# Optimization experiments

Hardware: AMD Instinct MI355X
Metric: run time of the kernel (lower is better)

## Reference

```python
import jax, jax.numpy as jnp
import numpy as np

B, S, D, L = 64, 512, 256, 3
NUM_BUCKETS = 1500  # RelativePositionBias default


def _ln(x, g, b):
    m = x.mean(-1, keepdims=True)
    v = x.var(-1, keepdims=True)
    return (x - m) * jax.lax.rsqrt(v + 1e-5) * g + b


def setup_inputs() -> dict:
    key = jax.random.key(0)
    ks = jax.random.split(key, 10)
    s = 0.02
    f32 = jnp.float32
    return dict(
        x=jax.random.normal(ks[0], (B, S, D), f32),
        mask=jnp.ones((B, S), jnp.int32),
        bias_table=jax.random.normal(ks[1], (NUM_BUCKETS,), f32) * s,  # n_heads=1
        ln_g=jnp.ones((L, D), f32), ln_b=jnp.zeros((L, D), f32),
        wq=jax.random.normal(ks[2], (L, D, D), f32) * s, bq=jnp.zeros((L, D), f32),
        wk=jax.random.normal(ks[3], (L, D, D), f32) * s, bk=jnp.zeros((L, D), f32),
        wv=jax.random.normal(ks[4], (L, D, D), f32) * s, bv=jnp.zeros((L, D), f32),
        wo=jax.random.normal(ks[5], (L, D, D), f32) * s, bo=jnp.zeros((L, D), f32),
        cm_ln_g=jnp.ones((L, D), f32), cm_ln_b=jnp.zeros((L, D), f32),
        w1=jax.random.normal(ks[6], (L, D, D), f32) * s, b1=jnp.zeros((L, D), f32),
        w2=jax.random.normal(ks[7], (L, D, D), f32) * s, b2=jnp.zeros((L, D), f32),
    )


def reference(x, mask, bias_table, ln_g, ln_b, wq, bq, wk, bk, wv, bv, wo, bo,
              cm_ln_g, cm_ln_b, w1, b1, w2, b2):
    slen = x.shape[1]
    # relative position bias (RelativePositionBias.compute_bias), n_heads=1
    pos = jnp.arange(slen)
    rel = pos[None, :] - pos[:, None]        # memory - context
    maxn = slen - 1                          # torch.max(rel)
    bucket = jnp.where(rel < 0, -rel + maxn, rel)
    cp = bias_table[bucket]                  # [S, S], broadcasts over batch
    scale = jnp.sqrt(jnp.asarray(x.shape[-1], x.dtype))  # sqrt(hid_dim // 1)
    pad = (mask == 0)[:, None, :]            # [B, 1, S] key-side padding mask
    neg = jnp.finfo(x.dtype).min
    for j in range(L):
        h = _ln(x, ln_g[j], ln_b[j])
        q = h @ wq[j] + bq[j]
        k = h @ wk[j] + bk[j]
        v = h @ wv[j] + bv[j]
        e = jnp.einsum('bqd,bkd->bqk', q, k) / scale + cp
        e = jnp.where(pad, neg, e)
        a = jax.nn.softmax(e, axis=-1)
        o = jnp.einsum('bqk,bkd->bqd', a, v) @ wo[j] + bo[j]
        x = h + _ln(o, ln_g[j], ln_b[j])     # same LayerNorm reused, per source
        c = _ln(x, cm_ln_g[j], cm_ln_b[j])
        x = x + (jax.nn.gelu(c @ w1[j] + b1[j], approximate=False) @ w2[j] + b2[j])
    return x
```

## Files before the change

kernel.cpp:

```cpp
#include <hip/hip_runtime.h>
#include <hip/hip_bf16.h>
#include <math.h>

#define D_HID 256
#define N_B   64
#define S_LEN 512
#define N_L   3
#define M_ROWS (N_B * S_LEN)

typedef __bf16 bf16_t;
typedef __bf16 bf16x8 __attribute__((ext_vector_type(8)));
typedef __bf16 bf16x4 __attribute__((ext_vector_type(4)));
typedef float  f32x4  __attribute__((ext_vector_type(4)));
typedef unsigned int u32;

__device__ __forceinline__ f32x4 mfma16(bf16x8 a, bf16x8 b, f32x4 c) {
    return __builtin_amdgcn_mfma_f32_16x16x32_bf16(a, b, c, 0, 0, 0);
}

__device__ __forceinline__ void gld_lds16(const void* g, void* l) {
    __builtin_amdgcn_global_load_lds((const __attribute__((address_space(1))) u32*)g,
                                     (__attribute__((address_space(3))) u32*)l, 16, 0, 0);
}

__device__ __forceinline__ u32 pk_bf16(float a, float b) {
    return (u32)(__hip_bfloat16_raw(__hip_bfloat16(a)).x) |
           ((u32)(__hip_bfloat16_raw(__hip_bfloat16(b)).x) << 16);
}

__global__ __launch_bounds__(256) void transpose_all(const float* __restrict__ wq,
                                                     const float* __restrict__ wk,
                                                     const float* __restrict__ wv,
                                                     const float* __restrict__ wo,
                                                     const float* __restrict__ w1,
                                                     const float* __restrict__ w2,
                                                     bf16_t* __restrict__ Wqkv,
                                                     bf16_t* __restrict__ Wrest) {
    const int t = blockIdx.y;
    const float* src = t == 0 ? wq : t == 1 ? wk : t == 2 ? wv
                     : t == 3 ? wo : t == 4 ? w1 : w2;
    const int i = blockIdx.x * 256 + threadIdx.x;
    const int k = i & 255;
    const int n = (i >> 8) & 255;
    const int l = i >> 16;
    const bf16_t v = (bf16_t)src[((size_t)l << 16) + ((size_t)k << 8) + n];
    if (t < 3) Wqkv[(size_t)l * 3 * 65536 + t * 65536 + n * 256 + k] = v;
    else       Wrest[(size_t)(t - 3) * 196608 + l * 65536 + n * 256 + k] = v;
}

__global__ __launch_bounds__(256) void ln_fwd(const float* __restrict__ in,
                                              const float* __restrict__ g,
                                              const float* __restrict__ b,
                                              float* __restrict__ H,
                                              bf16_t* __restrict__ Hb) {
    int row  = blockIdx.x * 4 + (threadIdx.x >> 6);
    int lane = threadIdx.x & 63;
    float4 x = ((const float4*)(in + (size_t)row * D_HID))[lane];
    float s  = x.x + x.y + x.z + x.w;
    float sq = x.x * x.x + x.y * x.y + x.z * x.z + x.w * x.w;
#pragma unroll
    for (int o = 1; o < 64; o <<= 1) { s += __shfl_xor(s, o); sq += __shfl_xor(sq, o); }
    float mean = s * (1.f / D_HID);
    float rstd = rsqrtf(sq * (1.f / D_HID) - mean * mean + 1e-5f);
    float4 gv = ((const float4*)g)[lane];
    float4 bv = ((const float4*)b)[lane];
    float4 h;
    h.x = (x.x - mean) * rstd * gv.x + bv.x;
    h.y = (x.y - mean) * rstd * gv.y + bv.y;
    h.z = (x.z - mean) * rstd * gv.z + bv.z;
    h.w = (x.w - mean) * rstd * gv.w + bv.w;
    ((float4*)(H + (size_t)row * D_HID))[lane] = h;
    bf16x4 hb = { (bf16_t)h.x, (bf16_t)h.y, (bf16_t)h.z, (bf16_t)h.w };
    *((bf16x4*)(Hb + (size_t)row * D_HID) + lane) = hb;
}

__global__ __launch_bounds__(256) void ln_res_ln(const float* __restrict__ T,
                                                 const float* __restrict__ H,
                                                 const float* __restrict__ g,
                                                 const float* __restrict__ b,
                                                 const float* __restrict__ cg,
                                                 const float* __restrict__ cb,
                                                 float* __restrict__ X,
                                                 bf16_t* __restrict__ Cb) {
    int row  = blockIdx.x * 4 + (threadIdx.x >> 6);
    int lane = threadIdx.x & 63;
    float4 t = ((const float4*)(T + (size_t)row * D_HID))[lane];
    float s  = t.x + t.y + t.z + t.w;
    float sq = t.x * t.x + t.y * t.y + t.z * t.z + t.w * t.w;
#pragma unroll
    for (int o = 1; o < 64; o <<= 1) { s += __shfl_xor(s, o); sq += __shfl_xor(sq, o); }
    float mean = s * (1.f / D_HID);
    float rstd = rsqrtf(sq * (1.f / D_HID) - mean * mean + 1e-5f);
    float4 gv = ((const float4*)g)[lane];
    float4 bv = ((const float4*)b)[lane];
    float4 hh = ((const float4*)(H + (size_t)row * D_HID))[lane];
    float4 x;
    x.x = hh.x + (t.x - mean) * rstd * gv.x + bv.x;
    x.y = hh.y + (t.y - mean) * rstd * gv.y + bv.y;
    x.z = hh.z + (t.z - mean) * rstd * gv.z + bv.z;
    x.w = hh.w + (t.w - mean) * rstd * gv.w + bv.w;
    ((float4*)(X + (size_t)row * D_HID))[lane] = x;
    float s2  = x.x + x.y + x.z + x.w;
    float sq2 = x.x * x.x + x.y * x.y + x.z * x.z + x.w * x.w;
#pragma unroll
    for (int o = 1; o < 64; o <<= 1) { s2 += __shfl_xor(s2, o); sq2 += __shfl_xor(sq2, o); }
    float mean2 = s2 * (1.f / D_HID);
    float rstd2 = rsqrtf(sq2 * (1.f / D_HID) - mean2 * mean2 + 1e-5f);
    float4 cgv = ((const float4*)cg)[lane];
    float4 cbv = ((const float4*)cb)[lane];
    bf16x4 c = { (bf16_t)((x.x - mean2) * rstd2 * cgv.x + cbv.x),
                 (bf16_t)((x.y - mean2) * rstd2 * cgv.y + cbv.y),
                 (bf16_t)((x.z - mean2) * rstd2 * cgv.z + cbv.z),
                 (bf16_t)((x.w - mean2) * rstd2 * cgv.w + cbv.w) };
    *((bf16x4*)(Cb + (size_t)row * D_HID) + lane) = c;
}

__device__ __forceinline__ void stage_tile(const bf16_t* __restrict__ A,
                                           const bf16_t* __restrict__ W,
                                           int m0, int n0, int kt,
                                           bf16_t* As, bf16_t* Bs) {
    const int lane = threadIdx.x & 63;
    const int wid  = threadIdx.x >> 6;
#pragma unroll
    for (int i = 0; i < 4; ++i) {
        const int base8 = i * 256 + wid * 64;
        const int idx8  = base8 + lane;
        const int row   = idx8 >> 3;
        const int sc8   = (idx8 & 7) ^ (row & 7);
        gld_lds16(A + (size_t)(m0 + row) * D_HID + kt * 64 + sc8 * 8, As + base8 * 8);
        gld_lds16(W + (size_t)(n0 + row) * D_HID + kt * 64 + sc8 * 8, Bs + base8 * 8);
    }
}

__device__ __forceinline__ void compute_tile(const bf16_t* As, const bf16_t* Bs,
                                             f32x4 (&acc)[4][4]) {
    const int lane = threadIdx.x & 63;
    const int wid  = threadIdx.x >> 6;
    const int wm = wid >> 1, wn = wid & 1;
    const int r = lane & 15, g = lane >> 4;
#pragma unroll
    for (int ks = 0; ks < 2; ++ks) {
        bf16x8 af[4], bfr[4];
#pragma unroll
        for (int mt = 0; mt < 4; ++mt) {
            const int row = wm * 64 + mt * 16 + r;
            const int c8  = (ks * 4 + g) ^ (row & 7);
            af[mt] = *(const bf16x8*)(As + row * 64 + c8 * 8);
        }
#pragma unroll
        for (int nt = 0; nt < 4; ++nt) {
            const int row = wn * 64 + nt * 16 + r;
            const int c8  = (ks * 4 + g) ^ (row & 7);
            bfr[nt] = *(const bf16x8*)(Bs + row * 64 + c8 * 8);
        }
#pragma unroll
        for (int mt = 0; mt < 4; ++mt)
#pragma unroll
            for (int nt = 0; nt < 4; ++nt)
                acc[mt][nt] = mfma16(af[mt], bfr[nt], acc[mt][nt]);
    }
}

__device__ __forceinline__ void gemm_core(const bf16_t* __restrict__ A,
                                          const bf16_t* __restrict__ W,
                                          int m0, int n0,
                                          bf16_t (&As)[2][8192], bf16_t (&Bs)[2][8192],
                                          f32x4 (&acc)[4][4]) {
    stage_tile(A, W, m0, n0, 0, As[0], Bs[0]);
    asm volatile("s_waitcnt vmcnt(0)" ::: "memory");
    __builtin_amdgcn_s_barrier();
#pragma unroll
    for (int kt = 0; kt < 4; ++kt) {
        const int cur = kt & 1;
        if (kt < 3) stage_tile(A, W, m0, n0, kt + 1, As[cur ^ 1], Bs[cur ^ 1]);
        compute_tile(As[cur], Bs[cur], acc);
        if (kt < 3) {
            asm volatile("s_waitcnt vmcnt(0)" ::: "memory");
            __builtin_amdgcn_s_barrier();
        }
    }
}

__global__ __launch_bounds__(256) void gemm_qkv(const bf16_t* __restrict__ A,
                                                const bf16_t* __restrict__ Wp,
                                                const float* __restrict__ bq,
                                                const float* __restrict__ bk,
                                                const float* __restrict__ bv,
                                                bf16_t* __restrict__ Qb,
                                                bf16_t* __restrict__ Kb,
                                                bf16_t* __restrict__ Vt) {
    __shared__ bf16_t As[2][8192], Bs[2][8192];
    f32x4 acc[4][4] = {};
    const int m0 = blockIdx.x * 128, n0 = blockIdx.y * 128;
    gemm_core(A, Wp, m0, n0, As, Bs, acc);
    const int lane = threadIdx.x & 63, wid = threadIdx.x >> 6;
    const int wm = wid >> 1, wn = wid & 1, r = lane & 15, g = lane >> 4;
#pragma unroll
    for (int nt = 0; nt < 4; ++nt) {
        const int col = n0 + wn * 64 + nt * 16 + r;
        const int t = col >> 8, cc = col & 255;
        const float bias = (t == 0 ? bq : t == 1 ? bk : bv)[cc];
#pragma unroll
        for (int mt = 0; mt < 4; ++mt)
#pragma unroll
            for (int rr = 0; rr < 4; ++rr) {
                const int row = m0 + wm * 64 + mt * 16 + g * 4 + rr;
                const float v = acc[mt][nt][rr] + bias;
                if (t == 0)      Qb[(size_t)row * D_HID + cc] = (bf16_t)v;
                else if (t == 1) Kb[(size_t)row * D_HID + cc] = (bf16_t)v;
                else             Vt[((size_t)(row >> 9) * D_HID + cc) * S_LEN + (row & 511)] = (bf16_t)v;
            }
    }
}

template <int EPI>
__global__ __launch_bounds__(256) void gemm_one(const bf16_t* __restrict__ A,
                                                const bf16_t* __restrict__ W,
                                                const float* __restrict__ bias,
                                                void* __restrict__ outp,
                                                const float* __restrict__ addsrc) {
    __shared__ bf16_t As[2][8192], Bs[2][8192];
    f32x4 acc[4][4] = {};
    const int m0 = blockIdx.x * 128, n0 = blockIdx.y * 128;
    gemm_core(A, W, m0, n0, As, Bs, acc);
    const int lane = threadIdx.x & 63, wid = threadIdx.x >> 6;
    const int wm = wid >> 1, wn = wid & 1, r = lane & 15, g = lane >> 4;
#pragma unroll
    for (int nt = 0; nt < 4; ++nt) {
        const int col = n0 + wn * 64 + nt * 16 + r;
        const float bv = bias[col];
#pragma unroll
        for (int mt = 0; mt < 4; ++mt)
#pragma unroll
            for (int rr = 0; rr < 4; ++rr) {
                const size_t idx = (size_t)(m0 + wm * 64 + mt * 16 + g * 4 + rr) * D_HID + col;
                float v = acc[mt][nt][rr] + bv;
                if constexpr (EPI == 1) {
                    v = 0.5f * v * (1.f + erff(v * 0.70710678118654752f));
                    ((bf16_t*)outp)[idx] = (bf16_t)v;
                } else if constexpr (EPI == 2) {
                    ((float*)outp)[idx] = v;
                } else {
                    ((float*)outp)[idx] = addsrc[idx] + v;
                }
            }
    }
}

__global__ __launch_bounds__(256, 2) void attn_fwd(const bf16_t* __restrict__ Q,
                                                   const bf16_t* __restrict__ K,
                                                   const bf16_t* __restrict__ Vt,
                                                   const float* __restrict__ btab,
                                                   const int* __restrict__ mask,
                                                   bf16_t* __restrict__ AO) {
    __shared__ float  bias_lds[1024];
    __shared__ float  mask_add[512];
    __shared__ bf16_t P_lds[32 * 64];
    __shared__ float  m_part[4][32], l_part[4][32];
    __shared__ bf16_t o_lds[32][264];

    const int tid = threadIdx.x, lane = tid & 63, w = tid >> 6;
    const int r = lane & 15, g = lane >> 4;

    const int lid = blockIdx.x;
    const int xcd = lid & 7, slot = lid >> 3;
    const int b  = xcd * 8 + (slot >> 4);
    const int q0 = (slot & 15) * 32;

    for (int i = tid; i < 1024; i += 256) {
        const int rel = i - 512;
        const int bucket = (rel < 0) ? (511 - rel) : rel;
        bias_lds[i] = btab[bucket];
    }
    for (int i = tid; i < 512; i += 256)
        mask_add[i] = mask[b * S_LEN + i] ? 0.f : -3.0e38f;
    __syncthreads();

    const bf16_t* Qp = Q  + ((size_t)b * S_LEN + q0) * D_HID;
    const bf16_t* Kp = K  + (size_t)b * S_LEN * D_HID;
    const bf16_t* Vp = Vt + (size_t)b * D_HID * S_LEN;

    bf16x8 qf[2][8];
#pragma unroll
    for (int ks = 0; ks < 8; ++ks) {
        qf[0][ks] = *(const bf16x8*)(Qp + (size_t)r * D_HID + ks * 32 + g * 8);
        qf[1][ks] = *(const bf16x8*)(Qp + (size_t)(16 + r) * D_HID + ks * 32 + g * 8);
    }

    f32x4 oacc[4][2] = {};
    float m_run[2] = {-3.0e38f, -3.0e38f};
    float l_run[2] = {0.f, 0.f};

#pragma unroll 1
    for (int kt = 0; kt < 8; ++kt) {
        const int k0 = kt * 64;
        bf16x8 vpre[2][4];
#pragma unroll
        for (int ks = 0; ks < 2; ++ks)
#pragma unroll
            for (int nt = 0; nt < 4; ++nt)
                vpre[ks][nt] = *(const bf16x8*)(Vp + (size_t)(w * 64 + nt * 16 + r) * S_LEN
                                                     + k0 + ks * 32 + g * 8);
        f32x4 sacc[2] = {};
#pragma unroll
        for (int ks = 0; ks < 8; ++ks) {
            const int dk = ks * 32 + g * 8;
            bf16x8 kf = *(const bf16x8*)(Kp + (size_t)(k0 + w * 16 + r) * D_HID + dk);
            sacc[0] = mfma16(kf, qf[0][ks], sacc[0]);
            sacc[1] = mfma16(kf, qf[1][ks], sacc[1]);
        }
        float mx[2] = {-3.0e38f, -3.0e38f};
#pragma unroll
        for (int qb = 0; qb < 2; ++qb) {
            const int qg = q0 + qb * 16 + r;
#pragma unroll
            for (int rr = 0; rr < 4; ++rr) {
                const int kg = k0 + w * 16 + g * 4 + rr;
                float ev = sacc[qb][rr] * 0.0625f + bias_lds[kg - qg + 512] + mask_add[kg];
                sacc[qb][rr] = ev;
                mx[qb] = fmaxf(mx[qb], ev);
            }
            mx[qb] = fmaxf(mx[qb], __shfl_xor(mx[qb], 16));
            mx[qb] = fmaxf(mx[qb], __shfl_xor(mx[qb], 32));
        }
        if (g == 0) { m_part[w][r] = mx[0]; m_part[w][16 + r] = mx[1]; }
        __syncthreads();
        float mnew[2], fac[2];
#pragma unroll
        for (int qb = 0; qb < 2; ++qb) {
            const int q = qb * 16 + r;
            const float tm = fmaxf(fmaxf(m_part[0][q], m_part[1][q]),
                                   fmaxf(m_part[2][q], m_part[3][q]));
            mnew[qb] = fmaxf(m_run[qb], tm);
            fac[qb]  = __expf(m_run[qb] - mnew[qb]);
            m_run[qb] = mnew[qb];
        }
#pragma unroll
        for (int qb = 0; qb < 2; ++qb) {
            const float p0 = __expf(sacc[qb][0] - mnew[qb]);
            const float p1 = __expf(sacc[qb][1] - mnew[qb]);
            const float p2 = __expf(sacc[qb][2] - mnew[qb]);
            const float p3 = __expf(sacc[qb][3] - mnew[qb]);
            float ls = p0 + p1 + p2 + p3;
            ls += __shfl_xor(ls, 16);
            ls += __shfl_xor(ls, 32);
            if (g == 0) l_part[w][qb * 16 + r] = ls;
            const int q = qb * 16 + r;
            const int u = (2 * w + (g >> 1)) ^ (q & 7);
            uint2 pv; pv.x = pk_bf16(p0, p1); pv.y = pk_bf16(p2, p3);
            *(uint2*)((char*)P_lds + q * 128 + u * 16 + (g & 1) * 8) = pv;
        }
        __syncthreads();
#pragma unroll
        for (int qb = 0; qb < 2; ++qb) {
            const int q = qb * 16 + r;
            const float lt = l_part[0][q] + l_part[1][q] + l_part[2][q] + l_part[3][q];
            l_run[qb] = l_run[qb] * fac[qb] + lt;
        }
#pragma unroll
        for (int nt = 0; nt < 4; ++nt)
#pragma unroll
            for (int qb = 0; qb < 2; ++qb)
#pragma unroll
                for (int rr = 0; rr < 4; ++rr)
                    oacc[nt][qb][rr] *= fac[qb];
#pragma unroll
        for (int ks = 0; ks < 2; ++ks) {
            bf16x8 pf[2];
#pragma unroll
            for (int qb = 0; qb < 2; ++qb) {
                const int q = qb * 16 + r;
                const int u = (ks * 4 + g) ^ (q & 7);
                pf[qb] = *(const bf16x8*)((const char*)P_lds + q * 128 + u * 16);
            }
            __builtin_amdgcn_s_setprio(1);
#pragma unroll
            for (int nt = 0; nt < 4; ++nt) {
                oacc[nt][0] = mfma16(vpre[ks][nt], pf[0], oacc[nt][0]);
                oacc[nt][1] = mfma16(vpre[ks][nt], pf[1], oacc[nt][1]);
            }
            __builtin_amdgcn_s_setprio(0);
        }
    }
    const float inv_l[2] = { 1.f / fmaxf(l_run[0], 1e-30f),
                             1.f / fmaxf(l_run[1], 1e-30f) };
#pragma unroll
    for (int nt = 0; nt < 4; ++nt)
#pragma unroll
        for (int qb = 0; qb < 2; ++qb) {
            const int q = qb * 16 + r;
            const int d = w * 64 + nt * 16 + g * 4;
            bf16x4 ob = { (bf16_t)(oacc[nt][qb][0] * inv_l[qb]),
                          (bf16_t)(oacc[nt][qb][1] * inv_l[qb]),
                          (bf16_t)(oacc[nt][qb][2] * inv_l[qb]),
                          (bf16_t)(oacc[nt][qb][3] * inv_l[qb]) };
            *(bf16x4*)&o_lds[q][d] = ob;
        }
    __syncthreads();
    bf16_t* Op = AO + ((size_t)b * S_LEN + q0) * D_HID;
#pragma unroll
    for (int it = 0; it < 4; ++it) {
        const int idx = it * 256 + tid;
        const int row = idx >> 5, u = idx & 31;
        bf16x8 vv = *(const bf16x8*)&o_lds[row][u * 8];
        *(bf16x8*)(Op + (size_t)row * D_HID + u * 8) = vv;
    }
}

extern "C" void kernel_launch(void* const* d_in, const int* in_sizes, int n_in,
                              void* d_out, int out_size, void* d_ws, size_t ws_size,
                              hipStream_t stream) {
    const float* x_in = (const float*)d_in[0];
    const int*   mask = (const int*)d_in[1];
    const float* btab = (const float*)d_in[2];
    const float* ln_g = (const float*)d_in[3];
    const float* ln_b = (const float*)d_in[4];
    const float* wq = (const float*)d_in[5];
    const float* bq = (const float*)d_in[6];
    const float* wk = (const float*)d_in[7];
    const float* bk = (const float*)d_in[8];
    const float* wv = (const float*)d_in[9];
    const float* bv = (const float*)d_in[10];
    const float* wo = (const float*)d_in[11];
    const float* bo = (const float*)d_in[12];
    const float* cg = (const float*)d_in[13];
    const float* cb = (const float*)d_in[14];
    const float* w1 = (const float*)d_in[15];
    const float* b1 = (const float*)d_in[16];
    const float* w2 = (const float*)d_in[17];
    const float* b2 = (const float*)d_in[18];
    float* out = (float*)d_out;

    char* p = (char*)d_ws;
    const size_t F32SZ  = (size_t)M_ROWS * D_HID * sizeof(float);
    const size_t BF16SZ = (size_t)M_ROWS * D_HID * sizeof(bf16_t);
    float*  H  = (float*)p;  p += F32SZ;
    float*  X  = (float*)p;  p += F32SZ;
    bf16_t* Hb = (bf16_t*)p; p += BF16SZ;
    bf16_t* Qb = (bf16_t*)p; p += BF16SZ;
    bf16_t* Kb = (bf16_t*)p;
    float*  T  = (float*)Kb;
    bf16_t* T1b = Kb;
    p += BF16SZ;
    bf16_t* Vt = (bf16_t*)p; p += BF16SZ;
    bf16_t* Wqkv = (bf16_t*)p; p += (size_t)N_L * 768 * 256 * sizeof(bf16_t);
    bf16_t* Wrest = (bf16_t*)p;
    bf16_t* AO = Hb;
    bf16_t* Cb = Qb;

    transpose_all<<<dim3(768, 6), dim3(256), 0, stream>>>(wq, wk, wv, wo, w1, w2, Wqkv, Wrest);

    const dim3 gblk(256, 1, 1);
    const dim3 grid_qkv(M_ROWS / 128, 6, 1);
    const dim3 grid_one(M_ROWS / 128, 2, 1);

    for (int j = 0; j < N_L; ++j) {
        const bf16_t* WQKVj = Wqkv + (size_t)j * 3 * 65536;
        const bf16_t* WOt = Wrest + ((size_t)0 * N_L + j) * 65536;
        const bf16_t* W1t = Wrest + ((size_t)1 * N_L + j) * 65536;
        const bf16_t* W2t = Wrest + ((size_t)2 * N_L + j) * 65536;

        ln_fwd<<<dim3(M_ROWS / 4), gblk, 0, stream>>>(j == 0 ? x_in : X,
                                                      ln_g + j * D_HID, ln_b + j * D_HID, H, Hb);
        gemm_qkv<<<grid_qkv, gblk, 0, stream>>>(Hb, WQKVj, bq + j * D_HID, bk + j * D_HID,
                                                bv + j * D_HID, Qb, Kb, Vt);
        attn_fwd<<<dim3(N_B * 16, 1, 1), gblk, 0, stream>>>(Qb, Kb, Vt, btab, mask, AO);
        gemm_one<2><<<grid_one, gblk, 0, stream>>>(AO, WOt, bo + j * D_HID, T, nullptr);
        ln_res_ln<<<dim3(M_ROWS / 4), gblk, 0, stream>>>(T, H, ln_g + j * D_HID, ln_b + j * D_HID,
                                                         cg + j * D_HID, cb + j * D_HID, X, Cb);
        gemm_one<1><<<grid_one, gblk, 0, stream>>>(Cb, W1t, b1 + j * D_HID, T1b, nullptr);
        gemm_one<3><<<grid_one, gblk, 0, stream>>>(T1b, W2t, b2 + j * D_HID,
                                                   (j == N_L - 1) ? (void*)out : (void*)X, X);
    }
}
```

Baseline: 687.7 us.

## Shrink GEMM and attention tiles and drop fp32 LayerNorm residual copy

GEMM block tiles shrink from 128x128 to 64x128, and attention blocks now cover 16 query rows instead of 32. Both changes double the grid size and lower per-block registers and LDS, aiming for better occupancy and load balance. The fp32 H buffer is removed: the residual now reads the bf16 LayerNorm output, which cuts memory traffic but adds rounding error to the residual path. AO gets its own buffer because Hb is still needed later for the residual. Attention blocks now reuse each K/V tile across fewer queries, so K/V reads from global memory double.

```diff
diff --git a/kernel.cpp b/kernel.cpp
--- a/kernel.cpp
+++ b/kernel.cpp
@@ -51,7 +51,6 @@
 __global__ __launch_bounds__(256) void ln_fwd(const float* __restrict__ in,
                                               const float* __restrict__ g,
                                               const float* __restrict__ b,
-                                              float* __restrict__ H,
                                               bf16_t* __restrict__ Hb) {
     int row  = blockIdx.x * 4 + (threadIdx.x >> 6);
     int lane = threadIdx.x & 63;
@@ -64,18 +63,15 @@
     float rstd = rsqrtf(sq * (1.f / D_HID) - mean * mean + 1e-5f);
     float4 gv = ((const float4*)g)[lane];
     float4 bv = ((const float4*)b)[lane];
-    float4 h;
-    h.x = (x.x - mean) * rstd * gv.x + bv.x;
-    h.y = (x.y - mean) * rstd * gv.y + bv.y;
-    h.z = (x.z - mean) * rstd * gv.z + bv.z;
-    h.w = (x.w - mean) * rstd * gv.w + bv.w;
-    ((float4*)(H + (size_t)row * D_HID))[lane] = h;
-    bf16x4 hb = { (bf16_t)h.x, (bf16_t)h.y, (bf16_t)h.z, (bf16_t)h.w };
+    bf16x4 hb = { (bf16_t)((x.x - mean) * rstd * gv.x + bv.x),
+                  (bf16_t)((x.y - mean) * rstd * gv.y + bv.y),
+                  (bf16_t)((x.z - mean) * rstd * gv.z + bv.z),
+                  (bf16_t)((x.w - mean) * rstd * gv.w + bv.w) };
     *((bf16x4*)(Hb + (size_t)row * D_HID) + lane) = hb;
 }
 
 __global__ __launch_bounds__(256) void ln_res_ln(const float* __restrict__ T,
-                                                 const float* __restrict__ H,
+                                                 const bf16_t* __restrict__ Hb,
                                                  const float* __restrict__ g,
                                                  const float* __restrict__ b,
                                                  const float* __restrict__ cg,
@@ -93,12 +89,12 @@
     float rstd = rsqrtf(sq * (1.f / D_HID) - mean * mean + 1e-5f);
     float4 gv = ((const float4*)g)[lane];
     float4 bv = ((const float4*)b)[lane];
-    float4 hh = ((const float4*)(H + (size_t)row * D_HID))[lane];
+    bf16x4 hb = *((const bf16x4*)(Hb + (size_t)row * D_HID) + lane);
     float4 x;
-    x.x = hh.x + (t.x - mean) * rstd * gv.x + bv.x;
-    x.y = hh.y + (t.y - mean) * rstd * gv.y + bv.y;
-    x.z = hh.z + (t.z - mean) * rstd * gv.z + bv.z;
-    x.w = hh.w + (t.w - mean) * rstd * gv.w + bv.w;
+    x.x = (float)hb[0] + (t.x - mean) * rstd * gv.x + bv.x;
+    x.y = (float)hb[1] + (t.y - mean) * rstd * gv.y + bv.y;
+    x.z = (float)hb[2] + (t.z - mean) * rstd * gv.z + bv.z;
+    x.w = (float)hb[3] + (t.w - mean) * rstd * gv.w + bv.w;
     ((float4*)(X + (size_t)row * D_HID))[lane] = x;
     float s2  = x.x + x.y + x.z + x.w;
     float sq2 = x.x * x.x + x.y * x.y + x.z * x.z + x.w * x.w;
@@ -122,28 +118,35 @@
     const int lane = threadIdx.x & 63;
     const int wid  = threadIdx.x >> 6;
 #pragma unroll
+    for (int i = 0; i < 2; ++i) {
+        const int base8 = i * 256 + wid * 64;
+        const int idx8  = base8 + lane;
+        const int row   = idx8 >> 3;
+        const int sc8   = (idx8 & 7) ^ (row & 7);
+        gld_lds16(A + (size_t)(m0 + row) * D_HID + kt * 64 + sc8 * 8, As + base8 * 8);
+    }
+#pragma unroll
     for (int i = 0; i < 4; ++i) {
         const int base8 = i * 256 + wid * 64;
         const int idx8  = base8 + lane;
         const int row   = idx8 >> 3;
         const int sc8   = (idx8 & 7) ^ (row & 7);
-        gld_lds16(A + (size_t)(m0 + row) * D_HID + kt * 64 + sc8 * 8, As + base8 * 8);
         gld_lds16(W + (size_t)(n0 + row) * D_HID + kt * 64 + sc8 * 8, Bs + base8 * 8);
     }
 }
 
 __device__ __forceinline__ void compute_tile(const bf16_t* As, const bf16_t* Bs,
-                                             f32x4 (&acc)[4][4]) {
+                                             f32x4 (&acc)[2][4]) {
     const int lane = threadIdx.x & 63;
     const int wid  = threadIdx.x >> 6;
     const int wm = wid >> 1, wn = wid & 1;
     const int r = lane & 15, g = lane >> 4;
 #pragma unroll
     for (int ks = 0; ks < 2; ++ks) {
-        bf16x8 af[4], bfr[4];
-#pragma unroll
-        for (int mt = 0; mt < 4; ++mt) {
-            const int row = wm * 64 + mt * 16 + r;
+        bf16x8 af[2], bfr[4];
+#pragma unroll
+        for (int mt = 0; mt < 2; ++mt) {
+            const int row = wm * 32 + mt * 16 + r;
             const int c8  = (ks * 4 + g) ^ (row & 7);
             af[mt] = *(const bf16x8*)(As + row * 64 + c8 * 8);
         }
@@ -154,7 +157,7 @@
             bfr[nt] = *(const bf16x8*)(Bs + row * 64 + c8 * 8);
         }
 #pragma unroll
-        for (int mt = 0; mt < 4; ++mt)
+        for (int mt = 0; mt < 2; ++mt)
 #pragma unroll
             for (int nt = 0; nt < 4; ++nt)
                 acc[mt][nt] = mfma16(af[mt], bfr[nt], acc[mt][nt]);
@@ -164,8 +167,8 @@
 __device__ __forceinline__ void gemm_core(const bf16_t* __restrict__ A,
                                           const bf16_t* __restrict__ W,
                                           int m0, int n0,
-                                          bf16_t (&As)[2][8192], bf16_t (&Bs)[2][8192],
-                                          f32x4 (&acc)[4][4]) {
+                                          bf16_t (&As)[2][4096], bf16_t (&Bs)[2][8192],
+                                          f32x4 (&acc)[2][4]) {
     stage_tile(A, W, m0, n0, 0, As[0], Bs[0]);
     asm volatile("s_waitcnt vmcnt(0)" ::: "memory");
     __builtin_amdgcn_s_barrier();
@@ -189,9 +192,9 @@
                                                 bf16_t* __restrict__ Qb,
                                                 bf16_t* __restrict__ Kb,
                                                 bf16_t* __restrict__ Vt) {
-    __shared__ bf16_t As[2][8192], Bs[2][8192];
-    f32x4 acc[4][4] = {};
-    const int m0 = blockIdx.x * 128, n0 = blockIdx.y * 128;
+    __shared__ bf16_t As[2][4096], Bs[2][8192];
+    f32x4 acc[2][4] = {};
+    const int m0 = blockIdx.x * 64, n0 = blockIdx.y * 128;
     gemm_core(A, Wp, m0, n0, As, Bs, acc);
     const int lane = threadIdx.x & 63, wid = threadIdx.x >> 6;
     const int wm = wid >> 1, wn = wid & 1, r = lane & 15, g = lane >> 4;
@@ -201,10 +204,10 @@
         const int t = col >> 8, cc = col & 255;
         const float bias = (t == 0 ? bq : t == 1 ? bk : bv)[cc];
 #pragma unroll
-        for (int mt = 0; mt < 4; ++mt)
+        for (int mt = 0; mt < 2; ++mt)
 #pragma unroll
             for (int rr = 0; rr < 4; ++rr) {
-                const int row = m0 + wm * 64 + mt * 16 + g * 4 + rr;
+                const int row = m0 + wm * 32 + mt * 16 + g * 4 + rr;
                 const float v = acc[mt][nt][rr] + bias;
                 if (t == 0)      Qb[(size_t)row * D_HID + cc] = (bf16_t)v;
                 else if (t == 1) Kb[(size_t)row * D_HID + cc] = (bf16_t)v;
@@ -219,9 +222,9 @@
                                                 const float* __restrict__ bias,
                                                 void* __restrict__ outp,
                                                 const float* __restrict__ addsrc) {
-    __shared__ bf16_t As[2][8192], Bs[2][8192];
-    f32x4 acc[4][4] = {};
-    const int m0 = blockIdx.x * 128, n0 = blockIdx.y * 128;
+    __shared__ bf16_t As[2][4096], Bs[2][8192];
+    f32x4 acc[2][4] = {};
+    const int m0 = blockIdx.x * 64, n0 = blockIdx.y * 128;
     gemm_core(A, W, m0, n0, As, Bs, acc);
     const int lane = threadIdx.x & 63, wid = threadIdx.x >> 6;
     const int wm = wid >> 1, wn = wid & 1, r = lane & 15, g = lane >> 4;
@@ -230,10 +233,10 @@
         const int col = n0 + wn * 64 + nt * 16 + r;
         const float bv = bias[col];
 #pragma unroll
-        for (int mt = 0; mt < 4; ++mt)
+        for (int mt = 0; mt < 2; ++mt)
 #pragma unroll
             for (int rr = 0; rr < 4; ++rr) {
-                const size_t idx = (size_t)(m0 + wm * 64 + mt * 16 + g * 4 + rr) * D_HID + col;
+                const size_t idx = (size_t)(m0 + wm * 32 + mt * 16 + g * 4 + rr) * D_HID + col;
                 float v = acc[mt][nt][rr] + bv;
                 if constexpr (EPI == 1) {
                     v = 0.5f * v * (1.f + erff(v * 0.70710678118654752f));
@@ -255,17 +258,17 @@
                                                    bf16_t* __restrict__ AO) {
     __shared__ float  bias_lds[1024];
     __shared__ float  mask_add[512];
-    __shared__ bf16_t P_lds[32 * 64];
-    __shared__ float  m_part[4][32], l_part[4][32];
-    __shared__ bf16_t o_lds[32][264];
+    __shared__ bf16_t P_lds[16 * 64];
+    __shared__ float  m_part[4][16], l_part[4][16];
+    __shared__ bf16_t o_lds[16][264];
 
     const int tid = threadIdx.x, lane = tid & 63, w = tid >> 6;
     const int r = lane & 15, g = lane >> 4;
 
     const int lid = blockIdx.x;
     const int xcd = lid & 7, slot = lid >> 3;
-    const int b  = xcd * 8 + (slot >> 4);
-    const int q0 = (slot & 15) * 32;
+    const int b  = xcd * 8 + (slot >> 5);
+    const int q0 = (slot & 31) * 16;
 
     for (int i = tid; i < 1024; i += 256) {
         const int rel = i - 512;
@@ -280,16 +283,13 @@
     const bf16_t* Kp = K  + (size_t)b * S_LEN * D_HID;
     const bf16_t* Vp = Vt + (size_t)b * D_HID * S_LEN;
 
-    bf16x8 qf[2][8];
-#pragma unroll
-    for (int ks = 0; ks < 8; ++ks) {
-        qf[0][ks] = *(const bf16x8*)(Qp + (size_t)r * D_HID + ks * 32 + g * 8);
-        qf[1][ks] = *(const bf16x8*)(Qp + (size_t)(16 + r) * D_HID + ks * 32 + g * 8);
-    }
-
-    f32x4 oacc[4][2] = {};
-    float m_run[2] = {-3.0e38f, -3.0e38f};
-    float l_run[2] = {0.f, 0.f};
+    bf16x8 qf[8];
+#pragma unroll
+    for (int ks = 0; ks < 8; ++ks)
+        qf[ks] = *(const bf16x8*)(Qp + (size_t)r * D_HID + ks * 32 + g * 8);
+
+    f32x4 oacc[4] = {};
+    float m_run = -3.0e38f, l_run = 0.f;
 
 #pragma unroll 1
     for (int kt = 0; kt < 8; ++kt) {
@@ -301,105 +301,76 @@
             for (int nt = 0; nt < 4; ++nt)
                 vpre[ks][nt] = *(const bf16x8*)(Vp + (size_t)(w * 64 + nt * 16 + r) * S_LEN
                                                      + k0 + ks * 32 + g * 8);
-        f32x4 sacc[2] = {};
+        f32x4 sacc = {};
 #pragma unroll
         for (int ks = 0; ks < 8; ++ks) {
-            const int dk = ks * 32 + g * 8;
-            bf16x8 kf = *(const bf16x8*)(Kp + (size_t)(k0 + w * 16 + r) * D_HID + dk);
-            sacc[0] = mfma16(kf, qf[0][ks], sacc[0]);
-            sacc[1] = mfma16(kf, qf[1][ks], sacc[1]);
-        }
-        float mx[2] = {-3.0e38f, -3.0e38f};
-#pragma unroll
-        for (int qb = 0; qb < 2; ++qb) {
-            const int qg = q0 + qb * 16 + r;
-#pragma unroll
-            for (int rr = 0; rr < 4; ++rr) {
-                const int kg = k0 + w * 16 + g * 4 + rr;
-                float ev = sacc[qb][rr] * 0.0625f + bias_lds[kg - qg + 512] + mask_add[kg];
-                sacc[qb][rr] = ev;
-                mx[qb] = fmaxf(mx[qb], ev);
-            }
-            mx[qb] = fmaxf(mx[qb], __shfl_xor(mx[qb], 16));
-            mx[qb] = fmaxf(mx[qb], __shfl_xor(mx[qb], 32));
-        }
-        if (g == 0) { m_part[w][r] = mx[0]; m_part[w][16 + r] = mx[1]; }
+            bf16x8 kf = *(const bf16x8*)(Kp + (size_t)(k0 + w * 16 + r) * D_HID + ks * 32 + g * 8);
+            sacc = mfma16(kf, qf[ks], sacc);
+        }
+        float mx = -3.0e38f;
+        const int qg = q0 + r;
+#pragma unroll
+        for (int rr = 0; rr < 4; ++rr) {
+            const int kg = k0 + w * 16 + g * 4 + rr;
+            float ev = sacc[rr] * 0.0625f + bias_lds[kg - qg + 512] + mask_add[kg];
+            sacc[rr] = ev;
+            mx = fmaxf(mx, ev);
+        }
+        mx = fmaxf(mx, __shfl_xor(mx, 16));
+        mx = fmaxf(mx, __shfl_xor(mx, 32));
+        if (g == 0) m_part[w][r] = mx;
         __syncthreads();
-        float mnew[2], fac[2];
-#pragma unroll
-        for (int qb = 0; qb < 2; ++qb) {
-            const int q = qb * 16 + r;
-            const float tm = fmaxf(fmaxf(m_part[0][q], m_part[1][q]),
-                                   fmaxf(m_part[2][q], m_part[3][q]));
-            mnew[qb] = fmaxf(m_run[qb], tm);
-            fac[qb]  = __expf(m_run[qb] - mnew[qb]);
-            m_run[qb] = mnew[qb];
-        }
-#pragma unroll
-        for (int qb = 0; qb < 2; ++qb) {
-            const float p0 = __expf(sacc[qb][0] - mnew[qb]);
-            const float p1 = __expf(sacc[qb][1] - mnew[qb]);
-            const float p2 = __expf(sacc[qb][2] - mnew[qb]);
-            const float p3 = __expf(sacc[qb][3] - mnew[qb]);
-            float ls = p0 + p1 + p2 + p3;
-            ls += __shfl_xor(ls, 16);
-            ls += __shfl_xor(ls, 32);
-            if (g == 0) l_part[w][qb * 16 + r] = ls;
-            const int q = qb * 16 + r;
-            const int u = (2 * w + (g >> 1)) ^ (q & 7);
+        const float tm = fmaxf(fmaxf(m_part[0][r], m_part[1][r]),
+                               fmaxf(m_part[2][r], m_part[3][r]));
+        const float mnew = fmaxf(m_run, tm);
+        const float fac  = __expf(m_run - mnew);
+        m_run = mnew;
+        const float p0 = __expf(sacc[0] - mnew);
+        const float p1 = __expf(sacc[1] - mnew);
+        const float p2 = __expf(sacc[2] - mnew);
+        const float p3 = __expf(sacc[3] - mnew);
+        float ls = p0 + p1 + p2 + p3;
+        ls += __shfl_xor(ls, 16);
+        ls += __shfl_xor(ls, 32);
+        if (g == 0) l_part[w][r] = ls;
+        {
+            const int u = (2 * w + (g >> 1)) ^ (r & 7);
             uint2 pv; pv.x = pk_bf16(p0, p1); pv.y = pk_bf16(p2, p3);
-            *(uint2*)((char*)P_lds + q * 128 + u * 16 + (g & 1) * 8) = pv;
+            *(uint2*)((char*)P_lds + r * 128 + u * 16 + (g & 1) * 8) = pv;
         }
         __syncthreads();
-#pragma unroll
-        for (int qb = 0; qb < 2; ++qb) {
-            const int q = qb * 16 + r;
-            const float lt = l_part[0][q] + l_part[1][q] + l_part[2][q] + l_part[3][q];
-            l_run[qb] = l_run[qb] * fac[qb] + lt;
-        }
+        const float lt = l_part[0][r] + l_part[1][r] + l_part[2][r] + l_part[3][r];
+        l_run = l_run * fac + lt;
 #pragma unroll
         for (int nt = 0; nt < 4; ++nt)
 #pragma unroll
-            for (int qb = 0; qb < 2; ++qb)
-#pragma unroll
-                for (int rr = 0; rr < 4; ++rr)
-                    oacc[nt][qb][rr] *= fac[qb];
+            for (int rr = 0; rr < 4; ++rr)
+                oacc[nt][rr] *= fac;
 #pragma unroll
         for (int ks = 0; ks < 2; ++ks) {
-            bf16x8 pf[2];
-#pragma unroll
-            for (int qb = 0; qb < 2; ++qb) {
-                const int q = qb * 16 + r;
-                const int u = (ks * 4 + g) ^ (q & 7);
-                pf[qb] = *(const bf16x8*)((const char*)P_lds + q * 128 + u * 16);
-            }
+            const int u = (ks * 4 + g) ^ (r & 7);
+            bf16x8 pf = *(const bf16x8*)((const char*)P_lds + r * 128 + u * 16);
             __builtin_amdgcn_s_setprio(1);
 #pragma unroll
-            for (int nt = 0; nt < 4; ++nt) {
-                oacc[nt][0] = mfma16(vpre[ks][nt], pf[0], oacc[nt][0]);
-                oacc[nt][1] = mfma16(vpre[ks][nt], pf[1], oacc[nt][1]);
-            }
+            for (int nt = 0; nt < 4; ++nt)
+                oacc[nt] = mfma16(vpre[ks][nt], pf, oacc[nt]);
             __builtin_amdgcn_s_setprio(0);
         }
     }
-    const float inv_l[2] = { 1.f / fmaxf(l_run[0], 1e-30f),
-                             1.f / fmaxf(l_run[1], 1e-30f) };
-#pragma unroll
-    for (int nt = 0; nt < 4; ++nt)
-#pragma unroll
-        for (int qb = 0; qb < 2; ++qb) {
-            const int q = qb * 16 + r;
-            const int d = w * 64 + nt * 16 + g * 4;
-            bf16x4 ob = { (bf16_t)(oacc[nt][qb][0] * inv_l[qb]),
-                          (bf16_t)(oacc[nt][qb][1] * inv_l[qb]),
-                          (bf16_t)(oacc[nt][qb][2] * inv_l[qb]),
-                          (bf16_t)(oacc[nt][qb][3] * inv_l[qb]) };
-            *(bf16x4*)&o_lds[q][d] = ob;
-        }
+    const float inv_l = 1.f / fmaxf(l_run, 1e-30f);
+#pragma unroll
+    for (int nt = 0; nt < 4; ++nt) {
+        const int d = w * 64 + nt * 16 + g * 4;
+        bf16x4 ob = { (bf16_t)(oacc[nt][0] * inv_l),
+                      (bf16_t)(oacc[nt][1] * inv_l),
+                      (bf16_t)(oacc[nt][2] * inv_l),
+                      (bf16_t)(oacc[nt][3] * inv_l) };
+        *(bf16x4*)&o_lds[r][d] = ob;
+    }
     __syncthreads();
     bf16_t* Op = AO + ((size_t)b * S_LEN + q0) * D_HID;
 #pragma unroll
-    for (int it = 0; it < 4; ++it) {
+    for (int it = 0; it < 2; ++it) {
         const int idx = it * 256 + tid;
         const int row = idx >> 5, u = idx & 31;
         bf16x8 vv = *(const bf16x8*)&o_lds[row][u * 8];
@@ -434,7 +405,6 @@
     char* p = (char*)d_ws;
     const size_t F32SZ  = (size_t)M_ROWS * D_HID * sizeof(float);
     const size_t BF16SZ = (size_t)M_ROWS * D_HID * sizeof(bf16_t);
-    float*  H  = (float*)p;  p += F32SZ;
     float*  X  = (float*)p;  p += F32SZ;
     bf16_t* Hb = (bf16_t*)p; p += BF16SZ;
     bf16_t* Qb = (bf16_t*)p; p += BF16SZ;
@@ -443,16 +413,16 @@
     bf16_t* T1b = Kb;
     p += BF16SZ;
     bf16_t* Vt = (bf16_t*)p; p += BF16SZ;
+    bf16_t* AO = (bf16_t*)p; p += BF16SZ;
     bf16_t* Wqkv = (bf16_t*)p; p += (size_t)N_L * 768 * 256 * sizeof(bf16_t);
     bf16_t* Wrest = (bf16_t*)p;
-    bf16_t* AO = Hb;
     bf16_t* Cb = Qb;
 
     transpose_all<<<dim3(768, 6), dim3(256), 0, stream>>>(wq, wk, wv, wo, w1, w2, Wqkv, Wrest);
 
     const dim3 gblk(256, 1, 1);
-    const dim3 grid_qkv(M_ROWS / 128, 6, 1);
-    const dim3 grid_one(M_ROWS / 128, 2, 1);
+    const dim3 grid_qkv(M_ROWS / 64, 6, 1);
+    const dim3 grid_one(M_ROWS / 64, 2, 1);
 
     for (int j = 0; j < N_L; ++j) {
         const bf16_t* WQKVj = Wqkv + (size_t)j * 3 * 65536;
@@ -461,12 +431,12 @@
         const bf16_t* W2t = Wrest + ((size_t)2 * N_L + j) * 65536;
 
         ln_fwd<<<dim3(M_ROWS / 4), gblk, 0, stream>>>(j == 0 ? x_in : X,
-                                                      ln_g + j * D_HID, ln_b + j * D_HID, H, Hb);
+                                                      ln_g + j * D_HID, ln_b + j * D_HID, Hb);
         gemm_qkv<<<grid_qkv, gblk, 0, stream>>>(Hb, WQKVj, bq + j * D_HID, bk + j * D_HID,
                                                 bv + j * D_HID, Qb, Kb, Vt);
-        attn_fwd<<<dim3(N_B * 16, 1, 1), gblk, 0, stream>>>(Qb, Kb, Vt, btab, mask, AO);
+        attn_fwd<<<dim3(N_B * 32, 1, 1), gblk, 0, stream>>>(Qb, Kb, Vt, btab, mask, AO);
         gemm_one<2><<<grid_one, gblk, 0, stream>>>(AO, WOt, bo + j * D_HID, T, nullptr);
-        ln_res_ln<<<dim3(M_ROWS / 4), gblk, 0, stream>>>(T, H, ln_g + j * D_HID, ln_b + j * D_HID,
+        ln_res_ln<<<dim3(M_ROWS / 4), gblk, 0, stream>>>(T, Hb, ln_g + j * D_HID, ln_b + j * D_HID,
                                                          cg + j * D_HID, cb + j * D_HID, X, Cb);
         gemm_one<1><<<grid_one, gblk, 0, stream>>>(Cb, W1t, b1 + j * D_HID, T1b, nullptr);
         gemm_one<3><<<grid_one, gblk, 0, stream>>>(T1b, W2t, b2 + j * D_HID,
```

Result: slower. 813.0 us (+18.2%).
